# Optimization experiments

Measured on AMD Instinct MI355X. Metric: run time of the kernel, lower is better.

## Reference

```python
import jax, jax.numpy as jnp
import numpy as np

N = 100000          # nodes
E = 1600000         # edges
H = 128             # hidden_size
V = 128             # num_activities
L = 3               # num_layers
G = 1024            # num graphs (pooling segments)


def setup_inputs() -> dict:
    key = jax.random.key(0)
    k0, k1, k2, k3, k4, k5 = jax.random.split(key, 6)
    x = jax.random.randint(k0, (N,), 0, V)
    edge_index = jax.random.randint(k1, (2, E), 0, N)
    batch = jnp.sort(jax.random.randint(k2, (N,), 0, G))
    emb_table = jax.random.normal(k3, (V, H), dtype=jnp.float32)
    Ws = jax.random.normal(k4, (L, H, H), dtype=jnp.float32) / np.sqrt(H).astype(np.float32)
    bs = jax.random.normal(k5, (L, H), dtype=jnp.float32) * 0.01
    return {"x": x, "edge_index": edge_index, "batch": batch,
            "emb_table": emb_table, "Ws": Ws, "bs": bs}


def _gcn_norm(edge_index):
    # add self loops, compute symmetric normalization D^-1/2 (A+I) D^-1/2
    loop = jnp.arange(N)
    src = jnp.concatenate([edge_index[0], loop])
    dst = jnp.concatenate([edge_index[1], loop])
    deg = jax.ops.segment_sum(jnp.ones_like(src, dtype=jnp.float32), dst, num_segments=N)
    dinv = jnp.where(deg > 0, jax.lax.rsqrt(jnp.maximum(deg, 1e-12)), 0.0)
    norm = dinv[src] * dinv[dst]  # [E+N]
    return src, dst, norm


def _gcn_forward(h, src, dst, norm, Ws, bs):
    for i in range(L):
        hw = h @ Ws[i]                                  # [N,H] linear
        msg = hw[src] * norm[:, None]                   # [E+N,H] gather + scale
        h = jax.ops.segment_sum(msg, dst, num_segments=N) + bs[i]
        if i < L - 1:
            h = jax.nn.relu(h)   # dropout(0.1) disabled at inference
    return h


def reference(x, edge_index, batch, emb_table, Ws, bs):
    h = emb_table[x]                                    # embedding lookup [N,H]
    src, dst, norm = _gcn_norm(edge_index)
    h = _gcn_forward(h, src, dst, norm, Ws, bs)
    # scatter_mean pooling over graph ids
    sums = jax.ops.segment_sum(h, batch, num_segments=G)
    cnts = jax.ops.segment_sum(jnp.ones((N,), dtype=h.dtype), batch, num_segments=G)
    return sums / jnp.maximum(cnts, 1.0)[:, None]       # [G,H]
```

## Files before the change

### kernel.cpp

```cpp
#include <hip/hip_runtime.h>

#define NN 100000
#define NE 1600000
#define HD 128
#define NL 3
#define NG 1024
#define CAP 64

typedef __attribute__((ext_vector_type(8))) short short8v;
typedef __attribute__((ext_vector_type(4))) float float4v;

__device__ inline unsigned short f2bf(float f) {
    unsigned int u = __float_as_uint(f);
    u += 0x7fffu + ((u >> 16) & 1u);
    return (unsigned short)(u >> 16);
}
__device__ inline float bf2f(unsigned short h) {
    return __uint_as_float(((unsigned int)h) << 16);
}
__device__ inline float2 bfpair(unsigned int u) {
    float2 r;
    r.x = __uint_as_float(u << 16);
    r.y = __uint_as_float(u & 0xffff0000u);
    return r;
}

__global__ void k_init(int* cnt, int* gstart, int* gend) {
    int i = blockIdx.x * blockDim.x + threadIdx.x;
    if (i < NN) cnt[i] = 0;
    if (i < NG) { gstart[i] = 0x7fffffff; gend[i] = 0; }
}

__global__ void k_fillcap(const int* __restrict__ src, const int* __restrict__ dst,
                          int* __restrict__ cnt, int* __restrict__ srcT) {
    int e = blockIdx.x * blockDim.x + threadIdx.x;
    if (e < NE) {
        int s = src[e], d = dst[e];
        int pos = atomicAdd(&cnt[d], 1);
        if (pos < CAP) srcT[d * CAP + pos] = s;
    }
}

__global__ void k_deg(const int* __restrict__ cnt, float* __restrict__ dinv) {
    int i = blockIdx.x * blockDim.x + threadIdx.x;
    if (i < NN) dinv[i] = rsqrtf((float)(cnt[i] + 1));
}

__global__ void k_wprep(const float* __restrict__ Ws,
                        unsigned short* __restrict__ WhT,
                        unsigned short* __restrict__ WlT) {
    int i = blockIdx.x * blockDim.x + threadIdx.x;
    if (i < NL * HD * HD) {
        int k = i & (HD - 1);
        int n = (i >> 7) & (HD - 1);
        int l = i >> 14;
        float f = Ws[(size_t)l * HD * HD + (size_t)k * HD + n];
        unsigned short hi = f2bf(f);
        WhT[i] = hi;
        WlT[i] = f2bf(f - bf2f(hi));
    }
}

template<int WITH_EMB>
__global__ __launch_bounds__(256) void k_gemm_mfma(const unsigned short* __restrict__ A,
                                                   const int* __restrict__ xidx,
                                                   const float* __restrict__ emb,
                                                   const unsigned short* __restrict__ WhT,
                                                   const unsigned short* __restrict__ WlT,
                                                   unsigned short* __restrict__ B) {
    __shared__ unsigned short Ah[64][40];
    __shared__ unsigned short Wh[128][40];
    __shared__ unsigned short Wl[128][40];
    __shared__ int xs[64];
    int n0 = blockIdx.x * 64;
    int t  = threadIdx.x;
    if (WITH_EMB && t < 64) xs[t] = (n0 + t < NN) ? xidx[n0 + t] : 0;
    int lane = t & 63, wv = t >> 6;
    int lm = lane & 15, lk = lane >> 4;
    float4v acc[8];
#pragma unroll
    for (int i = 0; i < 8; ++i) acc[i] = (float4v)0.f;

    for (int kc = 0; kc < 4; ++kc) {
        int k0 = kc * 32;
        __syncthreads();
        {
            int row = t >> 2, seg = t & 3;
            int r = n0 + row;
            uint4 u = make_uint4(0u, 0u, 0u, 0u);
            if (r < NN) {
                if (WITH_EMB) {
                    const float* p = emb + (size_t)xs[row] * HD + k0 + seg * 8;
                    float4 f0 = *(const float4*)p;
                    float4 f1 = *(const float4*)(p + 4);
                    u.x = (unsigned)f2bf(f0.x) | ((unsigned)f2bf(f0.y) << 16);
                    u.y = (unsigned)f2bf(f0.z) | ((unsigned)f2bf(f0.w) << 16);
                    u.z = (unsigned)f2bf(f1.x) | ((unsigned)f2bf(f1.y) << 16);
                    u.w = (unsigned)f2bf(f1.z) | ((unsigned)f2bf(f1.w) << 16);
                } else {
                    u = *(const uint4*)(A + (size_t)r * HD + k0 + seg * 8);
                }
            }
            *(uint4*)&Ah[row][seg * 8] = u;
        }
#pragma unroll
        for (int it = 0; it < 2; ++it) {
            int lin = t + it * 256;
            int n = lin >> 2, seg = lin & 3;
            *(uint4*)&Wh[n][seg * 8] =
                *(const uint4*)(WhT + (size_t)n * HD + k0 + seg * 8);
            *(uint4*)&Wl[n][seg * 8] =
                *(const uint4*)(WlT + (size_t)n * HD + k0 + seg * 8);
        }
        __syncthreads();
        short8v a = *(const short8v*)&Ah[wv * 16 + lm][lk * 8];
#pragma unroll
        for (int nt = 0; nt < 8; ++nt) {
            short8v bh = *(const short8v*)&Wh[nt * 16 + lm][lk * 8];
            short8v bl = *(const short8v*)&Wl[nt * 16 + lm][lk * 8];
            acc[nt] = __builtin_amdgcn_mfma_f32_16x16x32_bf16(a, bh, acc[nt], 0, 0, 0);
            acc[nt] = __builtin_amdgcn_mfma_f32_16x16x32_bf16(a, bl, acc[nt], 0, 0, 0);
        }
    }
    int rbase = n0 + wv * 16 + (lane >> 4) * 4;
#pragma unroll
    for (int nt = 0; nt < 8; ++nt) {
        int col = nt * 16 + lm;
#pragma unroll
        for (int rg = 0; rg < 4; ++rg) {
            int r = rbase + rg;
            if (r < NN) B[(size_t)r * HD + col] = f2bf(acc[nt][rg]);
        }
    }
}

__global__ __launch_bounds__(256) void k_gather(const unsigned short* __restrict__ B,
                                                const int* __restrict__ cnt,
                                                const int* __restrict__ srcT,
                                                const float* __restrict__ dinv,
                                                const float* __restrict__ bias,
                                                unsigned short* __restrict__ A, int relu) {
    int wid  = (blockIdx.x * blockDim.x + threadIdx.x) >> 6;
    int lane = threadIdx.x & 63;
    if (wid >= NN) return;
    int n = wid;
    float dn = dinv[n];
    float2 b0 = bfpair(*(const unsigned int*)(B + (size_t)n * HD + lane * 2));
    float2 acc;
    acc.x = dn * b0.x;
    acc.y = dn * b0.y;
    int end = cnt[n];
    if (end > CAP) end = CAP;
    const int* row = srcT + n * CAP;
    int idx = 0;
    if (end >= 8) {
        float wA[8]; unsigned int uA[8];
        {
            int s[8];
#pragma unroll
            for (int q = 0; q < 8; ++q) s[q] = row[q];
#pragma unroll
            for (int q = 0; q < 8; ++q) wA[q] = dinv[s[q]];
#pragma unroll
            for (int q = 0; q < 8; ++q)
                uA[q] = *(const unsigned int*)(B + (size_t)s[q] * HD + lane * 2);
        }
        int next = 8;
        while (next + 8 <= end) {
            float wB[8]; unsigned int uB[8];
            {
                int s[8];
#pragma unroll
                for (int q = 0; q < 8; ++q) s[q] = row[next + q];
#pragma unroll
                for (int q = 0; q < 8; ++q) wB[q] = dinv[s[q]];
#pragma unroll
                for (int q = 0; q < 8; ++q)
                    uB[q] = *(const unsigned int*)(B + (size_t)s[q] * HD + lane * 2);
            }
#pragma unroll
            for (int q = 0; q < 8; ++q) {
                float2 v = bfpair(uA[q]);
                acc.x = fmaf(wA[q], v.x, acc.x);
                acc.y = fmaf(wA[q], v.y, acc.y);
            }
#pragma unroll
            for (int q = 0; q < 8; ++q) { wA[q] = wB[q]; uA[q] = uB[q]; }
            next += 8;
        }
#pragma unroll
        for (int q = 0; q < 8; ++q) {
            float2 v = bfpair(uA[q]);
            acc.x = fmaf(wA[q], v.x, acc.x);
            acc.y = fmaf(wA[q], v.y, acc.y);
        }
        idx = next;
    }
    for (; idx < end; ++idx) {
        int s   = row[idx];
        float w = dinv[s];
        float2 v = bfpair(*(const unsigned int*)(B + (size_t)s * HD + lane * 2));
        acc.x = fmaf(w, v.x, acc.x);
        acc.y = fmaf(w, v.y, acc.y);
    }
    float2 bb = ((const float2*)bias)[lane];
    acc.x = fmaf(dn, acc.x, bb.x);
    acc.y = fmaf(dn, acc.y, bb.y);
    if (relu) { acc.x = fmaxf(acc.x, 0.f); acc.y = fmaxf(acc.y, 0.f); }
    unsigned int o = (unsigned)f2bf(acc.x) | ((unsigned)f2bf(acc.y) << 16);
    *(unsigned int*)(A + (size_t)n * HD + lane * 2) = o;
}

__global__ void k_bounds(const int* __restrict__ batch, int* __restrict__ gstart,
                         int* __restrict__ gend) {
    int i = blockIdx.x * blockDim.x + threadIdx.x;
    if (i < NN) {
        int g = batch[i];
        atomicMin(&gstart[g], i);
        atomicMax(&gend[g], i + 1);
    }
}

__global__ __launch_bounds__(128) void k_pool(const unsigned short* __restrict__ A,
                                              const int* __restrict__ gstart,
                                              const int* __restrict__ gend,
                                              float* __restrict__ out) {
    int g = blockIdx.x;
    int t = threadIdx.x;
    int s = gstart[g], e = gend[g];
    float acc[8];
#pragma unroll
    for (int q = 0; q < 8; ++q) acc[q] = 0.f;
    int cntn = 0;
    if (s < e) {
        cntn = e - s;
        int n = s;
        for (; n + 8 <= e; n += 8) {
#pragma unroll
            for (int q = 0; q < 8; ++q)
                acc[q] += bf2f(A[(size_t)(n + q) * HD + t]);
        }
        for (; n < e; ++n) acc[0] += bf2f(A[(size_t)n * HD + t]);
    }
    float tot = ((acc[0] + acc[1]) + (acc[2] + acc[3])) +
                ((acc[4] + acc[5]) + (acc[6] + acc[7]));
    out[(size_t)g * HD + t] = tot / fmaxf((float)cntn, 1.f);
}

extern "C" void kernel_launch(void* const* d_in, const int* in_sizes, int n_in,
                              void* d_out, int out_size, void* d_ws, size_t ws_size,
                              hipStream_t stream) {
    const int*   x     = (const int*)d_in[0];
    const int*   ei    = (const int*)d_in[1];
    const int*   batch = (const int*)d_in[2];
    const float* emb   = (const float*)d_in[3];
    const float* Ws    = (const float*)d_in[4];
    const float* bs    = (const float*)d_in[5];
    float* out = (float*)d_out;

    const int* srcE = ei;
    const int* dstE = ei + NE;

    char* ws = (char*)d_ws;
    size_t off = 0;
    auto alloc = [&](size_t bytes) {
        size_t o = off;
        off = (off + bytes + 255) & ~(size_t)255;
        return o;
    };
    unsigned short* hA  = (unsigned short*)(ws + alloc((size_t)NN * HD * 2));
    unsigned short* hB  = (unsigned short*)(ws + alloc((size_t)NN * HD * 2));
    unsigned short* WhT = (unsigned short*)(ws + alloc((size_t)NL * HD * HD * 2));
    unsigned short* WlT = (unsigned short*)(ws + alloc((size_t)NL * HD * HD * 2));
    float* dinv   = (float*)(ws + alloc((size_t)NN * 4));
    int*   cnt    = (int*)  (ws + alloc((size_t)NN * 4));
    int*   srcT   = (int*)  (ws + alloc((size_t)NN * CAP * 4));
    int*   gstart = (int*)  (ws + alloc((size_t)NG * 4));
    int*   gend   = (int*)  (ws + alloc((size_t)NG * 4));
    (void)ws_size; (void)in_sizes; (void)n_in; (void)out_size;

    k_init<<<(NN + 255) / 256, 256, 0, stream>>>(cnt, gstart, gend);
    k_fillcap<<<(NE + 255) / 256, 256, 0, stream>>>(srcE, dstE, cnt, srcT);
    k_deg<<<(NN + 255) / 256, 256, 0, stream>>>(cnt, dinv);
    k_wprep<<<(NL * HD * HD + 255) / 256, 256, 0, stream>>>(Ws, WhT, WlT);

    const int GGRID = (NN + 63) / 64;
    for (int l = 0; l < NL; ++l) {
        size_t wo = (size_t)l * HD * HD;
        if (l == 0)
            k_gemm_mfma<1><<<GGRID, 256, 0, stream>>>(hA, x, emb, WhT + wo, WlT + wo, hB);
        else
            k_gemm_mfma<0><<<GGRID, 256, 0, stream>>>(hA, x, emb, WhT + wo, WlT + wo, hB);
        k_gather<<<(NN + 3) / 4, 256, 0, stream>>>(hB, cnt, srcT, dinv,
                                                   bs + (size_t)l * HD, hA,
                                                   (l < NL - 1) ? 1 : 0);
    }

    k_bounds<<<(NN + 255) / 256, 256, 0, stream>>>(batch, gstart, gend);
    k_pool<<<NG, 128, 0, stream>>>(hA, gstart, gend, out);
}
```

Before: 474.8 us.

## Fuse neighbor aggregation before GEMM per layer and unroll edge fill by two

Each GCN layer now aggregates first (A_hat·H) and then applies the weight matrix plus bias and ReLU in a single kernel, relying on linearity to reorder the two steps. This removes the intermediate HW buffer write and read and halves the launches per layer. Layer 0 gathers fp32 embedding rows directly through the x indices, which adds an extra indirection and wider loads. The aggregation now runs one wave per 16 nodes serially inside a 64-node block, so there is less parallelism to hide gather latency. The edge-fill kernel also handles two edges per thread.

```diff
diff --git a/kernel.cpp b/kernel.cpp
--- a/kernel.cpp
+++ b/kernel.cpp
@@ -34,10 +34,14 @@
 __global__ void k_fillcap(const int* __restrict__ src, const int* __restrict__ dst,
                           int* __restrict__ cnt, int* __restrict__ srcT) {
     int e = blockIdx.x * blockDim.x + threadIdx.x;
-    if (e < NE) {
-        int s = src[e], d = dst[e];
-        int pos = atomicAdd(&cnt[d], 1);
-        if (pos < CAP) srcT[d * CAP + pos] = s;
+    const int H = NE / 2;
+    if (e < H) {
+        int s0 = src[e],     d0 = dst[e];
+        int s1 = src[e + H], d1 = dst[e + H];
+        int p0 = atomicAdd(&cnt[d0], 1);
+        int p1 = atomicAdd(&cnt[d1], 1);
+        if (p0 < CAP) srcT[d0 * CAP + p0] = s0;
+        if (p1 < CAP) srcT[d1 * CAP + p1] = s1;
     }
 }
 
@@ -61,154 +65,161 @@
     }
 }
 
-template<int WITH_EMB>
-__global__ __launch_bounds__(256) void k_gemm_mfma(const unsigned short* __restrict__ A,
-                                                   const int* __restrict__ xidx,
-                                                   const float* __restrict__ emb,
-                                                   const unsigned short* __restrict__ WhT,
-                                                   const unsigned short* __restrict__ WlT,
-                                                   unsigned short* __restrict__ B) {
-    __shared__ unsigned short Ah[64][40];
+template<int L0>
+__global__ __launch_bounds__(256) void k_fused(const unsigned short* __restrict__ Hprev,
+                                               const int* __restrict__ xidx,
+                                               const float* __restrict__ emb,
+                                               const int* __restrict__ cnt,
+                                               const int* __restrict__ srcT,
+                                               const float* __restrict__ dinv,
+                                               const unsigned short* __restrict__ WhT,
+                                               const unsigned short* __restrict__ WlT,
+                                               const float* __restrict__ bias,
+                                               unsigned short* __restrict__ Hout,
+                                               int relu) {
+    __shared__ unsigned short Ah[64][136];
     __shared__ unsigned short Wh[128][40];
     __shared__ unsigned short Wl[128][40];
-    __shared__ int xs[64];
     int n0 = blockIdx.x * 64;
     int t  = threadIdx.x;
-    if (WITH_EMB && t < 64) xs[t] = (n0 + t < NN) ? xidx[n0 + t] : 0;
     int lane = t & 63, wv = t >> 6;
+
+    for (int i = 0; i < 16; ++i) {
+        int node = wv * 16 + i;
+        int n = n0 + node;
+        float2 acc = make_float2(0.f, 0.f);
+        if (n < NN) {
+            float dn = dinv[n];
+            float2 hv;
+            if (L0) {
+                int xv = xidx[n];
+                hv = *(const float2*)(emb + (size_t)xv * HD + lane * 2);
+            } else {
+                hv = bfpair(*(const unsigned int*)(Hprev + (size_t)n * HD + lane * 2));
+            }
+            acc.x = dn * hv.x;
+            acc.y = dn * hv.y;
+            int end = cnt[n];
+            if (end > CAP) end = CAP;
+            const int* row = srcT + n * CAP;
+            int idx = 0;
+            if (end >= 8) {
+                float wA[8]; float2 uA[8];
+                {
+                    int s[8];
+#pragma unroll
+                    for (int q = 0; q < 8; ++q) s[q] = row[q];
+#pragma unroll
+                    for (int q = 0; q < 8; ++q) wA[q] = dinv[s[q]];
+                    if (L0) {
+                        int xv2[8];
+#pragma unroll
+                        for (int q = 0; q < 8; ++q) xv2[q] = xidx[s[q]];
+#pragma unroll
+                        for (int q = 0; q < 8; ++q)
+                            uA[q] = *(const float2*)(emb + (size_t)xv2[q] * HD + lane * 2);
+                    } else {
+#pragma unroll
+                        for (int q = 0; q < 8; ++q)
+                            uA[q] = bfpair(*(const unsigned int*)(Hprev + (size_t)s[q] * HD + lane * 2));
+                    }
+                }
+                int next = 8;
+                while (next + 8 <= end) {
+                    float wB[8]; float2 uB[8];
+                    {
+                        int s[8];
+#pragma unroll
+                        for (int q = 0; q < 8; ++q) s[q] = row[next + q];
+#pragma unroll
+                        for (int q = 0; q < 8; ++q) wB[q] = dinv[s[q]];
+                        if (L0) {
+                            int xv2[8];
+#pragma unroll
+                            for (int q = 0; q < 8; ++q) xv2[q] = xidx[s[q]];
+#pragma unroll
+                            for (int q = 0; q < 8; ++q)
+                                uB[q] = *(const float2*)(emb + (size_t)xv2[q] * HD + lane * 2);
+                        } else {
+#pragma unroll
+                            for (int q = 0; q < 8; ++q)
+                                uB[q] = bfpair(*(const unsigned int*)(Hprev + (size_t)s[q] * HD + lane * 2));
+                        }
+                    }
+#pragma unroll
+                    for (int q = 0; q < 8; ++q) {
+                        acc.x = fmaf(wA[q], uA[q].x, acc.x);
+                        acc.y = fmaf(wA[q], uA[q].y, acc.y);
+                    }
+#pragma unroll
+                    for (int q = 0; q < 8; ++q) { wA[q] = wB[q]; uA[q] = uB[q]; }
+                    next += 8;
+                }
+#pragma unroll
+                for (int q = 0; q < 8; ++q) {
+                    acc.x = fmaf(wA[q], uA[q].x, acc.x);
+                    acc.y = fmaf(wA[q], uA[q].y, acc.y);
+                }
+                idx = next;
+            }
+            for (; idx < end; ++idx) {
+                int s   = row[idx];
+                float w = dinv[s];
+                float2 v;
+                if (L0) v = *(const float2*)(emb + (size_t)xidx[s] * HD + lane * 2);
+                else    v = bfpair(*(const unsigned int*)(Hprev + (size_t)s * HD + lane * 2));
+                acc.x = fmaf(w, v.x, acc.x);
+                acc.y = fmaf(w, v.y, acc.y);
+            }
+            acc.x *= dn;
+            acc.y *= dn;
+        }
+        unsigned int o = (unsigned)f2bf(acc.x) | ((unsigned)f2bf(acc.y) << 16);
+        *(unsigned int*)&Ah[node][lane * 2] = o;
+    }
+    __syncthreads();
+
     int lm = lane & 15, lk = lane >> 4;
-    float4v acc[8];
-#pragma unroll
-    for (int i = 0; i < 8; ++i) acc[i] = (float4v)0.f;
-
+    float4v accv[8];
+#pragma unroll
+    for (int i = 0; i < 8; ++i) accv[i] = (float4v)0.f;
     for (int kc = 0; kc < 4; ++kc) {
         int k0 = kc * 32;
-        __syncthreads();
-        {
-            int row = t >> 2, seg = t & 3;
-            int r = n0 + row;
-            uint4 u = make_uint4(0u, 0u, 0u, 0u);
-            if (r < NN) {
-                if (WITH_EMB) {
-                    const float* p = emb + (size_t)xs[row] * HD + k0 + seg * 8;
-                    float4 f0 = *(const float4*)p;
-                    float4 f1 = *(const float4*)(p + 4);
-                    u.x = (unsigned)f2bf(f0.x) | ((unsigned)f2bf(f0.y) << 16);
-                    u.y = (unsigned)f2bf(f0.z) | ((unsigned)f2bf(f0.w) << 16);
-                    u.z = (unsigned)f2bf(f1.x) | ((unsigned)f2bf(f1.y) << 16);
-                    u.w = (unsigned)f2bf(f1.z) | ((unsigned)f2bf(f1.w) << 16);
-                } else {
-                    u = *(const uint4*)(A + (size_t)r * HD + k0 + seg * 8);
-                }
-            }
-            *(uint4*)&Ah[row][seg * 8] = u;
-        }
 #pragma unroll
         for (int it = 0; it < 2; ++it) {
             int lin = t + it * 256;
-            int n = lin >> 2, seg = lin & 3;
-            *(uint4*)&Wh[n][seg * 8] =
-                *(const uint4*)(WhT + (size_t)n * HD + k0 + seg * 8);
-            *(uint4*)&Wl[n][seg * 8] =
-                *(const uint4*)(WlT + (size_t)n * HD + k0 + seg * 8);
+            int nn = lin >> 2, seg = lin & 3;
+            *(uint4*)&Wh[nn][seg * 8] =
+                *(const uint4*)(WhT + (size_t)nn * HD + k0 + seg * 8);
+            *(uint4*)&Wl[nn][seg * 8] =
+                *(const uint4*)(WlT + (size_t)nn * HD + k0 + seg * 8);
         }
         __syncthreads();
-        short8v a = *(const short8v*)&Ah[wv * 16 + lm][lk * 8];
+        short8v a = *(const short8v*)&Ah[wv * 16 + lm][k0 + lk * 8];
 #pragma unroll
         for (int nt = 0; nt < 8; ++nt) {
             short8v bh = *(const short8v*)&Wh[nt * 16 + lm][lk * 8];
             short8v bl = *(const short8v*)&Wl[nt * 16 + lm][lk * 8];
-            acc[nt] = __builtin_amdgcn_mfma_f32_16x16x32_bf16(a, bh, acc[nt], 0, 0, 0);
-            acc[nt] = __builtin_amdgcn_mfma_f32_16x16x32_bf16(a, bl, acc[nt], 0, 0, 0);
-        }
+            accv[nt] = __builtin_amdgcn_mfma_f32_16x16x32_bf16(a, bh, accv[nt], 0, 0, 0);
+            accv[nt] = __builtin_amdgcn_mfma_f32_16x16x32_bf16(a, bl, accv[nt], 0, 0, 0);
+        }
+        __syncthreads();
     }
     int rbase = n0 + wv * 16 + (lane >> 4) * 4;
 #pragma unroll
     for (int nt = 0; nt < 8; ++nt) {
         int col = nt * 16 + lm;
+        float bb = bias[col];
 #pragma unroll
         for (int rg = 0; rg < 4; ++rg) {
             int r = rbase + rg;
-            if (r < NN) B[(size_t)r * HD + col] = f2bf(acc[nt][rg]);
-        }
-    }
-}
-
-__global__ __launch_bounds__(256) void k_gather(const unsigned short* __restrict__ B,
-                                                const int* __restrict__ cnt,
-                                                const int* __restrict__ srcT,
-                                                const float* __restrict__ dinv,
-                                                const float* __restrict__ bias,
-                                                unsigned short* __restrict__ A, int relu) {
-    int wid  = (blockIdx.x * blockDim.x + threadIdx.x) >> 6;
-    int lane = threadIdx.x & 63;
-    if (wid >= NN) return;
-    int n = wid;
-    float dn = dinv[n];
-    float2 b0 = bfpair(*(const unsigned int*)(B + (size_t)n * HD + lane * 2));
-    float2 acc;
-    acc.x = dn * b0.x;
-    acc.y = dn * b0.y;
-    int end = cnt[n];
-    if (end > CAP) end = CAP;
-    const int* row = srcT + n * CAP;
-    int idx = 0;
-    if (end >= 8) {
-        float wA[8]; unsigned int uA[8];
-        {
-            int s[8];
-#pragma unroll
-            for (int q = 0; q < 8; ++q) s[q] = row[q];
-#pragma unroll
-            for (int q = 0; q < 8; ++q) wA[q] = dinv[s[q]];
-#pragma unroll
-            for (int q = 0; q < 8; ++q)
-                uA[q] = *(const unsigned int*)(B + (size_t)s[q] * HD + lane * 2);
-        }
-        int next = 8;
-        while (next + 8 <= end) {
-            float wB[8]; unsigned int uB[8];
-            {
-                int s[8];
-#pragma unroll
-                for (int q = 0; q < 8; ++q) s[q] = row[next + q];
-#pragma unroll
-                for (int q = 0; q < 8; ++q) wB[q] = dinv[s[q]];
-#pragma unroll
-                for (int q = 0; q < 8; ++q)
-                    uB[q] = *(const unsigned int*)(B + (size_t)s[q] * HD + lane * 2);
+            if (r < NN) {
+                float v = accv[nt][rg] + bb;
+                if (relu) v = fmaxf(v, 0.f);
+                Hout[(size_t)r * HD + col] = f2bf(v);
             }
-#pragma unroll
-            for (int q = 0; q < 8; ++q) {
-                float2 v = bfpair(uA[q]);
-                acc.x = fmaf(wA[q], v.x, acc.x);
-                acc.y = fmaf(wA[q], v.y, acc.y);
-            }
-#pragma unroll
-            for (int q = 0; q < 8; ++q) { wA[q] = wB[q]; uA[q] = uB[q]; }
-            next += 8;
-        }
-#pragma unroll
-        for (int q = 0; q < 8; ++q) {
-            float2 v = bfpair(uA[q]);
-            acc.x = fmaf(wA[q], v.x, acc.x);
-            acc.y = fmaf(wA[q], v.y, acc.y);
-        }
-        idx = next;
-    }
-    for (; idx < end; ++idx) {
-        int s   = row[idx];
-        float w = dinv[s];
-        float2 v = bfpair(*(const unsigned int*)(B + (size_t)s * HD + lane * 2));
-        acc.x = fmaf(w, v.x, acc.x);
-        acc.y = fmaf(w, v.y, acc.y);
-    }
-    float2 bb = ((const float2*)bias)[lane];
-    acc.x = fmaf(dn, acc.x, bb.x);
-    acc.y = fmaf(dn, acc.y, bb.y);
-    if (relu) { acc.x = fmaxf(acc.x, 0.f); acc.y = fmaxf(acc.y, 0.f); }
-    unsigned int o = (unsigned)f2bf(acc.x) | ((unsigned)f2bf(acc.y) << 16);
-    *(unsigned int*)(A + (size_t)n * HD + lane * 2) = o;
+        }
+    }
 }
 
 __global__ void k_bounds(const int* __restrict__ batch, int* __restrict__ gstart,
@@ -280,21 +291,19 @@
     (void)ws_size; (void)in_sizes; (void)n_in; (void)out_size;
 
     k_init<<<(NN + 255) / 256, 256, 0, stream>>>(cnt, gstart, gend);
-    k_fillcap<<<(NE + 255) / 256, 256, 0, stream>>>(srcE, dstE, cnt, srcT);
+    k_fillcap<<<(NE / 2 + 255) / 256, 256, 0, stream>>>(srcE, dstE, cnt, srcT);
     k_deg<<<(NN + 255) / 256, 256, 0, stream>>>(cnt, dinv);
     k_wprep<<<(NL * HD * HD + 255) / 256, 256, 0, stream>>>(Ws, WhT, WlT);
 
     const int GGRID = (NN + 63) / 64;
-    for (int l = 0; l < NL; ++l) {
-        size_t wo = (size_t)l * HD * HD;
-        if (l == 0)
-            k_gemm_mfma<1><<<GGRID, 256, 0, stream>>>(hA, x, emb, WhT + wo, WlT + wo, hB);
-        else
-            k_gemm_mfma<0><<<GGRID, 256, 0, stream>>>(hA, x, emb, WhT + wo, WlT + wo, hB);
-        k_gather<<<(NN + 3) / 4, 256, 0, stream>>>(hB, cnt, srcT, dinv,
-                                                   bs + (size_t)l * HD, hA,
-                                                   (l < NL - 1) ? 1 : 0);
-    }
+    k_fused<1><<<GGRID, 256, 0, stream>>>(nullptr, x, emb, cnt, srcT, dinv,
+                                          WhT, WlT, bs, hA, 1);
+    k_fused<0><<<GGRID, 256, 0, stream>>>(hA, x, emb, cnt, srcT, dinv,
+                                          WhT + (size_t)1 * HD * HD, WlT + (size_t)1 * HD * HD,
+                                          bs + 1 * HD, hB, 1);
+    k_fused<0><<<GGRID, 256, 0, stream>>>(hB, x, emb, cnt, srcT, dinv,
+                                          WhT + (size_t)2 * HD * HD, WlT + (size_t)2 * HD * HD,
+                                          bs + 2 * HD, hA, 0);
 
     k_bounds<<<(NN + 255) / 256, 256, 0, stream>>>(batch, gstart, gend);
     k_pool<<<NG, 128, 0, stream>>>(hA, gstart, gend, out);
```

Result: slower. 782.6 us (+64.8%).
